# Kernel optimization log

Hardware: AMD Instinct MI355X
Metric: run time of the kernel (lower is better)

The kernel has to match this reference:

```python
import jax, jax.numpy as jnp
import numpy as np

KS = 2       # kernel_size (pad (0,1,0,1)+unfold only tiles to HxW for k=2)
L = 2        # num_attn_blocks
NH = 4       # n_heads
C = 128      # latent_dim
DH = C // NH
SCALE = 1.0 / float(np.sqrt(DH))


def _ln(x, eps=1e-6):
    m = jnp.mean(x, axis=-1, keepdims=True)
    v = jnp.var(x, axis=-1, keepdims=True)
    return (x - m) * jax.lax.rsqrt(v + eps)


def setup_inputs() -> dict:
    key = jax.random.key(0)
    ks = jax.random.split(key, 24)
    B, Hd, Wd, upf = 2, 64, 96, 2
    d = {
        'feat_map': jax.random.normal(ks[0], (B, C, Hd, Wd), jnp.float32),
        'feat_map_up': jax.random.normal(ks[1], (B, C, Hd * upf, Wd * upf), jnp.float32),
    }
    shapes = {'ctx_ln_b': (L, C), 'q_w': (L, C, C), 'q_b': (L, C), 'k_w': (L, C, C), 'k_b': (L, C),
              'v_w': (L, C, C), 'v_b': (L, C), 'o_w': (L, C, C), 'o_b': (L, C),
              'fc1_w': (L, C, 4 * C), 'fc1_b': (L, 4 * C), 'fc2_w': (L, 4 * C, C), 'fc2_b': (L, C),
              'out1_w': (3 * C, 3 * C), 'out1_b': (3 * C,), 'out2_w': (3 * C, 1), 'out2_b': (1,)}
    for i, (n, shp) in enumerate(shapes.items()):
        d[n] = jax.random.normal(ks[2 + i], shp, jnp.float32) * 0.02
    d['ctx_ln_g'] = jnp.ones((L, C), jnp.float32)
    d['upsample_factor'] = 2
    return d


def _forward(feat_map, feat_map_up, ctx_ln_g, ctx_ln_b, q_w, q_b, k_w, k_b, v_w, v_b,
             o_w, o_b, fc1_w, fc1_b, fc2_w, fc2_b, out1_w, out1_b, out2_w, out2_b, upf):
    B, _, Hd, Wd = feat_map.shape
    Hu, Wu = Hd * upf, Wd * upf
    N, K2 = B * Hu * Wu, KS * KS
    rh = jnp.minimum((jnp.arange(Hu) // upf)[:, None] + jnp.arange(KS)[None, :], Hd - 1)  # (Hu,KS)
    rw = jnp.minimum((jnp.arange(Wu) // upf)[:, None] + jnp.arange(KS)[None, :], Wd - 1)  # (Wu,KS)
    ctx = feat_map[:, :, rh][:, :, :, :, rw]                      # (B,C,Hu,KS,Wu,KS)
    ctx = jnp.transpose(ctx, (0, 2, 4, 3, 5, 1)).reshape(N, K2, C)  # (N,K2,C)
    # ALiBi bias: -L1(|up pixel coord - upf*down window coord|), separable in y/x
    dy = -jnp.abs(jnp.arange(Hu)[:, None] - rh * upf).astype(jnp.float32)  # (Hu,KS)
    dx = -jnp.abs(jnp.arange(Wu)[:, None] - rw * upf).astype(jnp.float32)  # (Wu,KS)
    cd = (dy[:, None, :, None] + dx[None, :, None, :]).reshape(Hu * Wu, K2)
    cd = jnp.tile(cd, (B, 1))                                     # (N,K2)
    x24 = 24.0 ** (1.0 / NH)
    slopes = 1.0 / x24 ** (jnp.arange(NH, dtype=jnp.float32) + 1.0)
    bias = slopes[None, :, None, None] * cd[:, None, None, :]     # (N,NH,1,K2)

    x = jnp.transpose(feat_map_up, (0, 2, 3, 1)).reshape(N, 1, C)
    for l in range(L):
        xn = _ln(x)
        cn = _ln(ctx, eps=1e-5) * ctx_ln_g[l] + ctx_ln_b[l]
        q = (xn @ q_w[l] + q_b[l]).reshape(N, 1, NH, DH).transpose(0, 2, 1, 3)
        k = (cn @ k_w[l] + k_b[l]).reshape(N, K2, NH, DH).transpose(0, 2, 1, 3)
        v = (cn @ v_w[l] + v_b[l]).reshape(N, K2, NH, DH).transpose(0, 2, 1, 3)
        sim = jnp.einsum('nhqd,nhkd->nhqk', q, k) * SCALE + bias
        attn = jax.nn.softmax(sim, axis=-1)
        o = jnp.einsum('nhqk,nhkd->nhqd', attn, v).transpose(0, 2, 1, 3).reshape(N, 1, C)
        x = x + o @ o_w[l] + o_b[l]
        h = _ln(x)
        x = x + jax.nn.gelu(h @ fc1_w[l] + fc1_b[l], approximate=True) @ fc2_w[l] + fc2_b[l]

    xf = _ln(x)      # (N,1,C)
    cf = _ln(ctx)    # (N,K2,C)
    fin = jnp.concatenate([jnp.broadcast_to(xf, (N, K2, C)), cf, xf - cf], axis=-1)  # (N,K2,3C)
    h1 = jax.nn.gelu(fin @ out1_w + out1_b, approximate=False)
    out = (h1 @ out2_w + out2_b).reshape(B, Hu, Wu, K2).transpose(0, 3, 1, 2)  # (B,K2,Hu,Wu)
    return jax.nn.softmax(out, axis=1)


def reference(feat_map, feat_map_up, ctx_ln_b, q_w, q_b, k_w, k_b, v_w, v_b, o_w, o_b,
              fc1_w, fc1_b, fc2_w, fc2_b, out1_w, out1_b, out2_w, out2_b, ctx_ln_g,
              upsample_factor):
    return _forward(feat_map, feat_map_up, ctx_ln_g, ctx_ln_b, q_w, q_b, k_w, k_b,
                    v_w, v_b, o_w, o_b, fc1_w, fc1_b, fc2_w, fc2_b,
                    out1_w, out1_b, out2_w, out2_b, upsample_factor)
```

## Files before the change

### kernel.cpp

```cpp
#include <hip/hip_runtime.h>
#include <math.h>

#define C_   128
#define HU_  128
#define WU_  192
#define HD_  64
#define WD_  96
#define HWD_ (HD_ * WD_)

typedef unsigned short u16;
typedef __attribute__((ext_vector_type(8))) short s8v;
typedef __attribute__((ext_vector_type(4))) float f4v;

#define OFF_Q   0
#define OFF_K   32768
#define OFF_V   65536
#define OFF_O   98304
#define OFF_F1  131072
#define OFF_F2  262144
#define OFF_XC  393216
#define OFF_CC  442368
#define OFF_NRM 491520
#define OFF_VB  2064384

#define SLOT 2176

__device__ __forceinline__ u16 f2bf(float f) {
    unsigned u = __float_as_uint(f);
    unsigned r = (u + 0x7FFFu + ((u >> 16) & 1u)) >> 16;
    return (u16)r;
}
__device__ __forceinline__ float bfu(u16 h) { return __uint_as_float(((unsigned)h) << 16); }

__device__ __forceinline__ float gelu_tanh(float x) {
    float u = 1.5957691216057308f * (x + 0.044715f * x * x * x);
    float e = __expf(u);
    float th = 1.0f - 2.0f / (1.0f + e);
    return 0.5f * x * (1.0f + th);
}
__device__ __forceinline__ float fast_erf(float x) {
    float z = fabsf(x);
    float t = 1.0f / (1.0f + 0.3275911f * z);
    float p = t * (0.254829592f + t * (-0.284496736f + t * (1.421413741f +
              t * (-1.453152027f + t * 1.061405429f))));
    float r = 1.0f - p * __expf(-z * z);
    return copysignf(r, x);
}
__device__ __forceinline__ float gelu_erf(float x) {
    return 0.5f * x * (1.0f + fast_erf(x * 0.7071067811865476f));
}

__device__ __forceinline__ void glds1(const u16* src, u16* dst, int lane) {
    __builtin_amdgcn_global_load_lds(
        (const __attribute__((address_space(1))) void*)(src + (size_t)lane * 8),
        (__attribute__((address_space(3))) void*)dst, 16, 0, 0);
}
#define WAITVM8() asm volatile("s_waitcnt vmcnt(8)" ::: "memory")
#define WAITVM6() asm volatile("s_waitcnt vmcnt(6)" ::: "memory")
#define WAITVM0() asm volatile("s_waitcnt vmcnt(0)" ::: "memory")

__global__ __launch_bounds__(256) void swz_all(
    const float* __restrict__ q_w, const float* __restrict__ k_w,
    const float* __restrict__ v_w, const float* __restrict__ o_w,
    const float* __restrict__ f1w, const float* __restrict__ f2w,
    const float* __restrict__ o1w,
    const float* __restrict__ ctx_g, const float* __restrict__ ctx_b,
    const float* __restrict__ vb_in, u16* __restrict__ ws)
{
    int tid = blockIdx.x * 256 + threadIdx.x;
    int f = tid >> 6, lane = tid & 63;
    if (f >= 964) return;
    if (f >= 960) {
        int lf = f - 960;
        int ly = lf >> 1, col = (lf & 1) * 64 + lane;
        float s = vb_in[ly * 128 + col];
        const float* bp = ctx_b + ly * 128;
        const float* wp = v_w + (size_t)ly * 128 * 128 + col;
        for (int c = 0; c < 128; ++c) s += bp[c] * wp[(size_t)c * 128];
        ((float*)(ws + OFF_VB))[ly * 128 + col] = s;
        return;
    }
    int rq = 8 * (lane >> 4), cq = lane & 15;
    const float* src; const float* src2 = nullptr; float sgn = 1.f;
    int NT, N, dstoff, lf;
    bool scale_g = false;
    if (f < 64)       { src = q_w;  NT = 8;  N = 128; dstoff = OFF_Q;  lf = f; }
    else if (f < 128) { src = k_w;  NT = 8;  N = 128; dstoff = OFF_K;  lf = f - 64;  scale_g = true; }
    else if (f < 192) { src = v_w;  NT = 8;  N = 128; dstoff = OFF_V;  lf = f - 128; scale_g = true; }
    else if (f < 256) { src = o_w;  NT = 8;  N = 128; dstoff = OFF_O;  lf = f - 192; }
    else if (f < 512) { src = f1w;  NT = 32; N = 512; dstoff = OFF_F1; lf = f - 256; }
    else if (f < 768) { src = f2w;  NT = 8;  N = 128; dstoff = OFF_F2; lf = f - 512; }
    else if (f < 864) { src = o1w;             src2 = o1w + 256 * 384; sgn =  1.f;
                        NT = 24; N = 384; dstoff = OFF_XC; lf = f - 768; }
    else              { src = o1w + 128 * 384; src2 = o1w + 256 * 384; sgn = -1.f;
                        NT = 24; N = 384; dstoff = OFF_CC; lf = f - 864; }
    int kt = lf / NT, nt = lf - kt * NT;
    int row0 = kt * 32 + rq, col = nt * 16 + cq;
    s8v o;
#pragma unroll
    for (int j = 0; j < 8; ++j) {
        float v = src[(size_t)(row0 + j) * N + col];
        if (src2) v += sgn * src2[(size_t)(row0 + j) * N + col];
        if (scale_g) v *= ctx_g[row0 + j];
        o[j] = (short)f2bf(v);
    }
    *(s8v*)(ws + dstoff + (size_t)lf * 512 + (size_t)lane * 8) = o;
}

__global__ __launch_bounds__(256) void norm_kernel(const float* __restrict__ fm,
                                                   u16* __restrict__ dst) {
    int row = blockIdx.x;
    int b = row >> 6, y = row & 63;
    __shared__ float tile[128 * 97];
    __shared__ float smean[96], srst[96];
    for (int idx = threadIdx.x; idx < 128 * 96; idx += 256) {
        int c = idx / 96, w = idx - c * 96;
        tile[c * 97 + w] = fm[(((size_t)b * 128 + c) * 64 + y) * 96 + w];
    }
    __syncthreads();
    if (threadIdx.x < 96) {
        int w = threadIdx.x;
        float s = 0.f, ss = 0.f;
        for (int c = 0; c < 128; ++c) { float v = tile[c * 97 + w]; s += v; ss += v * v; }
        float mn = s * (1.f / 128.f);
        smean[w] = mn;
        srst[w]  = rsqrtf(ss * (1.f / 128.f) - mn * mn + 1e-5f);
    }
    __syncthreads();
    for (int idx = threadIdx.x; idx < 96 * 16; idx += 256) {
        int w = idx >> 4, cg = idx & 15;
        float mn = smean[w], iv = srst[w];
        s8v o;
#pragma unroll
        for (int j = 0; j < 8; ++j)
            o[j] = (short)f2bf((tile[(8 * cg + j) * 97 + w] - mn) * iv);
        *(s8v*)(dst + ((size_t)row * 96 + w) * 128 + 8 * cg) = o;
    }
}

__global__ __launch_bounds__(64, 2) void fused_kernel(
    const u16*  __restrict__ nrmb, const float* __restrict__ fmu,
    const u16*  __restrict__ wsb,
    const float* __restrict__ qb, const float* __restrict__ ob,
    const float* __restrict__ f1b, const float* __restrict__ f2b,
    const float* __restrict__ o1b, const float* __restrict__ o2w,
    const float* __restrict__ o2b,
    float* __restrict__ out)
{
    const int lane = threadIdx.x;
    const int cidx = lane & 15, quad = lane >> 4;
    const int n0 = blockIdx.x * 16;
    const int b  = n0 / (HU_ * WU_);
    const int rem = n0 - b * (HU_ * WU_);
    const int hu  = rem / WU_;
    const int wu0 = rem - hu * WU_;

    __shared__ __align__(16) u16 wlds[2][4096];
    __shared__ u16 arena[2 * SLOT];
    __shared__ float s_at[272];
    float* s_rs = s_at;

    const float* vbp = (const float*)(wsb + OFF_VB);

    float xacc[8][4];
#pragma unroll
    for (int nt = 0; nt < 8; ++nt) {
        int ch = 16 * nt + cidx;
        float4 v = *(const float4*)(fmu + ((size_t)(b * C_ + ch) * HU_ + hu) * WU_ + wu0 + 4 * quad);
        xacc[nt][0] = v.x; xacc[nt][1] = v.y; xacc[nt][2] = v.z; xacc[nt][3] = v.w;
    }

    const float slopes[4] = {0.451801007f, 0.204124145f, 0.092223264f, 0.041666668f};
    const int ry0 = min(hu >> 1, HD_ - 1);
    const int ry1 = min((hu >> 1) + 1, HD_ - 1);
    const float dyv0 = -(float)abs(hu - 2 * ry0);
    const float dyv1 = -(float)abs(hu - 2 * ry1);

    const int k2l = cidx & 3;
    const int ryl = (k2l >> 1) ? ry1 : ry0;
    int cbase[4];
#pragma unroll
    for (int mt = 0; mt < 4; ++mt) {
        int p = 4 * mt + (cidx >> 2);
        int rxv = min(((wu0 + p) >> 1) + (k2l & 1), WD_ - 1);
        cbase[mt] = ((b * HD_ + ryl) * WD_ + rxv) * 128;
    }

#pragma unroll 1
    for (int ly = 0; ly < 2; ++ly) {
        const u16* Wq = wsb + OFF_Q  + ly * 16384;
        const u16* Wk = wsb + OFF_K  + ly * 16384;
        const u16* Wv = wsb + OFF_V  + ly * 16384;
        const u16* Wo = wsb + OFF_O  + ly * 16384;
        const u16* W1 = wsb + OFF_F1 + ly * 65536;
        const u16* W2 = wsb + OFF_F2 + ly * 65536;

        s8v fr[4][2];

#pragma unroll
        for (int jj = 0; jj < 8; ++jj) glds1(Wq + (size_t)jj * 512, &wlds[0][jj * 512], lane);
#pragma unroll
        for (int jj = 0; jj < 8; ++jj) glds1(Wq + (size_t)(8 + jj) * 512, &wlds[1][jj * 512], lane);

        {
            float mo[4], io[4];
#pragma unroll
            for (int r = 0; r < 4; ++r) {
                float s = 0.f, ss = 0.f;
#pragma unroll
                for (int nt = 0; nt < 8; ++nt) { float v = xacc[nt][r]; s += v; ss += v * v; }
#pragma unroll
                for (int m = 1; m <= 8; m <<= 1) { s += __shfl_xor(s, m, 64); ss += __shfl_xor(ss, m, 64); }
                float mn = s * (1.f / 128.f);
                mo[r] = mn; io[r] = rsqrtf(ss * (1.f / 128.f) - mn * mn + 1e-6f);
            }
#pragma unroll
            for (int nt = 0; nt < 8; ++nt)
#pragma unroll
                for (int r = 0; r < 4; ++r)
                    arena[(4 * quad + r) * 136 + 16 * nt + cidx] =
                        f2bf((xacc[nt][r] - mo[r]) * io[r]);
        }
        __syncthreads();
        s8v a_xn[4];
#pragma unroll
        for (int kt = 0; kt < 4; ++kt)
            a_xn[kt] = *(const s8v*)(arena + cidx * 136 + kt * 32 + 8 * quad);

        {
            f4v qa[8];
#pragma unroll
            for (int nt = 0; nt < 8; ++nt) {
                float bvv = qb[ly * C_ + 16 * nt + cidx];
                f4v t = {bvv, bvv, bvv, bvv}; qa[nt] = t;
            }
#pragma unroll
            for (int g = 0; g < 4; ++g) {
                if (g < 3) { WAITVM8(); } else { WAITVM0(); }
#pragma unroll
                for (int nt = 0; nt < 8; ++nt) {
                    s8v w = *(const s8v*)&wlds[g & 1][nt * 512 + lane * 8];
                    qa[nt] = __builtin_amdgcn_mfma_f32_16x16x32_bf16(a_xn[g], w, qa[nt], 0, 0, 0);
                }
                if (g < 2) {
#pragma unroll
                    for (int jj = 0; jj < 8; ++jj)
                        glds1(Wq + (size_t)((g + 2) * 8 + jj) * 512, &wlds[g & 1][jj * 512], lane);
                }
            }
#pragma unroll
            for (int kt = 0; kt < 4; ++kt)
#pragma unroll
                for (int i = 0; i < 2; ++i)
                    fr[kt][i] = *(const s8v*)(nrmb + cbase[i] + kt * 32 + 8 * quad);
#pragma unroll
            for (int jj = 0; jj < 8; ++jj)
                glds1(Wk + (size_t)(((jj & 3) * 8) + (jj >> 2)) * 512, &wlds[0][jj * 512], lane);
#pragma unroll
            for (int jj = 0; jj < 8; ++jj) {
                const int j = 8 + jj;
                glds1(Wk + (size_t)(((j & 3) * 8) + (j >> 2)) * 512, &wlds[1][jj * 512], lane);
            }
#pragma unroll
            for (int nt = 0; nt < 8; ++nt)
#pragma unroll
                for (int r = 0; r < 4; ++r)
                    arena[(4 * quad + r) * 136 + 16 * nt + cidx] = f2bf(qa[nt][r]);
        }
        __syncthreads();

#pragma unroll
        for (int g = 0; g < 8; ++g) {
            if (g < 7) { WAITVM8(); } else { WAITVM0(); }
            if (g == 4) {
#pragma unroll
                for (int kt = 0; kt < 4; ++kt)
#pragma unroll
                    for (int i = 0; i < 2; ++i)
                        fr[kt][i] = *(const s8v*)(nrmb + cbase[2 + i] + kt * 32 + 8 * quad);
            }
            const int mh = g >> 2, h = g & 3;
            float part[2][4];
#pragma unroll
            for (int i = 0; i < 2; ++i)
#pragma unroll
                for (int r = 0; r < 4; ++r) part[i][r] = 0.f;
#pragma unroll
            for (int ntp = 0; ntp < 2; ++ntp) {
                const int nt = 2 * h + ntp;
                f4v ka[2];
#pragma unroll
                for (int i = 0; i < 2; ++i) { f4v t = {0.f, 0.f, 0.f, 0.f}; ka[i] = t; }
#pragma unroll
                for (int kt = 0; kt < 4; ++kt) {
                    s8v w = *(const s8v*)&wlds[g & 1][(ntp * 4 + kt) * 512 + lane * 8];
                    ka[0] = __builtin_amdgcn_mfma_f32_16x16x32_bf16(fr[kt][0], w, ka[0], 0, 0, 0);
                    ka[1] = __builtin_amdgcn_mfma_f32_16x16x32_bf16(fr[kt][1], w, ka[1], 0, 0, 0);
                }
#pragma unroll
                for (int i = 0; i < 2; ++i) {
                    float qv = bfu(arena[(4 * (2 * mh + i) + quad) * 136 + 16 * nt + cidx]);
#pragma unroll
                    for (int r = 0; r < 4; ++r) part[i][r] = fmaf(qv, ka[i][r], part[i][r]);
                }
            }
#pragma unroll
            for (int i = 0; i < 2; ++i)
#pragma unroll
                for (int r = 0; r < 4; ++r) {
#pragma unroll
                    for (int m = 1; m <= 8; m <<= 1) part[i][r] += __shfl_xor(part[i][r], m, 64);
                }
            if (cidx == 0) {
#pragma unroll
                for (int i = 0; i < 2; ++i) {
                    float4 t = {part[i][0], part[i][1], part[i][2], part[i][3]};
                    *(float4*)&s_at[(4 * (2 * mh + i) + quad) * 16 + 4 * h] = t;
                }
            }
            if (g < 6) {
                const int gn = g + 2;
#pragma unroll
                for (int jj = 0; jj < 8; ++jj) {
                    const int j = 8 * (gn & 3) + jj;
                    glds1(Wk + (size_t)(((j & 3) * 8) + (j >> 2)) * 512, &wlds[g & 1][jj * 512], lane);
                }
            }
        }
#pragma unroll
        for (int kt = 0; kt < 4; ++kt)
#pragma unroll
            for (int i = 0; i < 2; ++i)
                fr[kt][i] = *(const s8v*)(nrmb + cbase[i] + kt * 32 + 8 * quad);
#pragma unroll
        for (int jj = 0; jj < 8; ++jj)
            glds1(Wv + (size_t)(((jj & 3) * 8) + (jj >> 2)) * 512, &wlds[0][jj * 512], lane);
#pragma unroll
        for (int jj = 0; jj < 8; ++jj)
            glds1(Wv + (size_t)(((jj & 3) * 8) + 2 + (jj >> 2)) * 512, &wlds[1][jj * 512], lane);
        __syncthreads();

        {
            int p = lane >> 2, h = lane & 3;
            float4 sc = *(float4*)&s_at[p * 16 + 4 * h];
            int pw = wu0 + p;
            float sim[4] = {sc.x, sc.y, sc.z, sc.w};
#pragma unroll
            for (int r = 0; r < 4; ++r) {
                int rxv = min((pw >> 1) + (r & 1), WD_ - 1);
                float cd = ((r >> 1) ? dyv1 : dyv0) - (float)abs(pw - 2 * rxv);
                sim[r] = sim[r] * 0.17677669529663687f + slopes[h] * cd;
            }
            float mx = fmaxf(fmaxf(sim[0], sim[1]), fmaxf(sim[2], sim[3]));
            float e0 = __expf(sim[0] - mx), e1 = __expf(sim[1] - mx);
            float e2 = __expf(sim[2] - mx), e3 = __expf(sim[3] - mx);
            float si = 1.f / (e0 + e1 + e2 + e3);
            float4 at = {e0 * si, e1 * si, e2 * si, e3 * si};
            *(float4*)&s_at[p * 16 + 4 * h] = at;
        }
        __syncthreads();

#pragma unroll
        for (int g = 0; g < 8; ++g) {
            if (g < 7) { WAITVM8(); } else { WAITVM0(); }
            if (g == 4) {
#pragma unroll
                for (int kt = 0; kt < 4; ++kt)
#pragma unroll
                    for (int i = 0; i < 2; ++i)
                        fr[kt][i] = *(const s8v*)(nrmb + cbase[2 + i] + kt * 32 + 8 * quad);
            }
            const int mh = g >> 2, gp = g & 3;
#pragma unroll
            for (int ntp = 0; ntp < 2; ++ntp) {
                const int nt = 2 * gp + ntp;
                float vbb = vbp[ly * C_ + 16 * nt + cidx];
                f4v va[2];
#pragma unroll
                for (int i = 0; i < 2; ++i) { f4v t = {vbb, vbb, vbb, vbb}; va[i] = t; }
#pragma unroll
                for (int kt = 0; kt < 4; ++kt) {
                    s8v w = *(const s8v*)&wlds[g & 1][(ntp * 4 + kt) * 512 + lane * 8];
                    va[0] = __builtin_amdgcn_mfma_f32_16x16x32_bf16(fr[kt][0], w, va[0], 0, 0, 0);
                    va[1] = __builtin_amdgcn_mfma_f32_16x16x32_bf16(fr[kt][1], w, va[1], 0, 0, 0);
                }
                const int h = nt >> 1;
#pragma unroll
                for (int i = 0; i < 2; ++i) {
                    const int mt = 2 * mh + i;
                    float4 at = *(float4*)&s_at[(4 * mt + quad) * 16 + 4 * h];
                    float ov = at.x * va[i][0] + at.y * va[i][1] + at.z * va[i][2] + at.w * va[i][3];
                    arena[(4 * mt + quad) * 136 + 16 * nt + cidx] = f2bf(ov);
                }
            }
            if (g < 6) {
                const int gq = (g + 2) & 3;
#pragma unroll
                for (int jj = 0; jj < 8; ++jj)
                    glds1(Wv + (size_t)(((jj & 3) * 8) + 2 * gq + (jj >> 2)) * 512, &wlds[g & 1][jj * 512], lane);
            }
        }
#pragma unroll
        for (int jj = 0; jj < 8; ++jj) glds1(Wo + (size_t)jj * 512, &wlds[0][jj * 512], lane);
#pragma unroll
        for (int jj = 0; jj < 8; ++jj) glds1(Wo + (size_t)(8 + jj) * 512, &wlds[1][jj * 512], lane);
        __syncthreads();

        {
            s8v a_o[4];
#pragma unroll
            for (int kt = 0; kt < 4; ++kt)
                a_o[kt] = *(const s8v*)(arena + cidx * 136 + kt * 32 + 8 * quad);
            f4v oa[8];
#pragma unroll
            for (int nt = 0; nt < 8; ++nt) {
                float bvv = ob[ly * C_ + 16 * nt + cidx];
                f4v t = {bvv, bvv, bvv, bvv}; oa[nt] = t;
            }
#pragma unroll
            for (int g = 0; g < 4; ++g) {
                if (g < 3) { WAITVM8(); } else { WAITVM0(); }
#pragma unroll
                for (int nt = 0; nt < 8; ++nt) {
                    s8v w = *(const s8v*)&wlds[g & 1][nt * 512 + lane * 8];
                    oa[nt] = __builtin_amdgcn_mfma_f32_16x16x32_bf16(a_o[g], w, oa[nt], 0, 0, 0);
                }
                if (g < 2) {
#pragma unroll
                    for (int jj = 0; jj < 8; ++jj)
                        glds1(Wo + (size_t)((g + 2) * 8 + jj) * 512, &wlds[g & 1][jj * 512], lane);
                }
            }
#pragma unroll
            for (int jj = 0; jj < 8; ++jj) glds1(W1 + (size_t)jj * 512, &wlds[0][jj * 512], lane);
#pragma unroll
            for (int jj = 0; jj < 8; ++jj) glds1(W1 + (size_t)(32 + jj) * 512, &wlds[1][jj * 512], lane);
#pragma unroll
            for (int nt = 0; nt < 8; ++nt)
#pragma unroll
                for (int r = 0; r < 4; ++r) xacc[nt][r] += oa[nt][r];
        }
        __syncthreads();

        {
            float mo[4], io[4];
#pragma unroll
            for (int r = 0; r < 4; ++r) {
                float s = 0.f, ss = 0.f;
#pragma unroll
                for (int nt = 0; nt < 8; ++nt) { float v = xacc[nt][r]; s += v; ss += v * v; }
#pragma unroll
                for (int m = 1; m <= 8; m <<= 1) { s += __shfl_xor(s, m, 64); ss += __shfl_xor(ss, m, 64); }
                float mn = s * (1.f / 128.f);
                mo[r] = mn; io[r] = rsqrtf(ss * (1.f / 128.f) - mn * mn + 1e-6f);
            }
#pragma unroll
            for (int nt = 0; nt < 8; ++nt)
#pragma unroll
                for (int r = 0; r < 4; ++r)
                    arena[(4 * quad + r) * 136 + 16 * nt + cidx] =
                        f2bf((xacc[nt][r] - mo[r]) * io[r]);
        }
        __syncthreads();
        s8v a_hn[4];
#pragma unroll
        for (int kt = 0; kt < 4; ++kt)
            a_hn[kt] = *(const s8v*)(arena + cidx * 136 + kt * 32 + 8 * quad);

        {
            f4v ga[8];
#pragma unroll
            for (int nt = 0; nt < 8; ++nt) {
                float bvv = f2b[ly * C_ + 16 * nt + cidx];
                f4v t = {bvv, bvv, bvv, bvv}; ga[nt] = t;
            }
#pragma unroll 1
            for (int c = 0; c < 4; ++c) {
                f4v fa[8];
#pragma unroll
                for (int nt = 0; nt < 8; ++nt) {
                    float bvv = f1b[ly * 512 + 128 * c + 16 * nt + cidx];
                    f4v t = {bvv, bvv, bvv, bvv}; fa[nt] = t;
                }
#pragma unroll
                for (int g = 0; g < 4; ++g) {
                    if (g < 3) { WAITVM8(); } else { WAITVM0(); }
#pragma unroll
                    for (int nt = 0; nt < 8; ++nt) {
                        s8v w = *(const s8v*)&wlds[g & 1][nt * 512 + lane * 8];
                        fa[nt] = __builtin_amdgcn_mfma_f32_16x16x32_bf16(a_hn[g], w, fa[nt], 0, 0, 0);
                    }
                    if (g < 2) {
#pragma unroll
                        for (int jj = 0; jj < 8; ++jj)
                            glds1(W1 + (size_t)((g + 2) * 32 + 8 * c + jj) * 512, &wlds[g & 1][jj * 512], lane);
                    }
                }
#pragma unroll
                for (int jj = 0; jj < 8; ++jj)
                    glds1(W2 + (size_t)(32 * c + jj) * 512, &wlds[0][jj * 512], lane);
#pragma unroll
                for (int jj = 0; jj < 8; ++jj)
                    glds1(W2 + (size_t)(32 * c + 8 + jj) * 512, &wlds[1][jj * 512], lane);
#pragma unroll
                for (int nt = 0; nt < 8; ++nt)
#pragma unroll
                    for (int r = 0; r < 4; ++r)
                        arena[SLOT + (4 * quad + r) * 136 + 16 * nt + cidx] =
                            f2bf(gelu_tanh(fa[nt][r]));
                __syncthreads();
#pragma unroll
                for (int g = 0; g < 4; ++g) {
                    if (g < 3) { WAITVM8(); } else { WAITVM0(); }
                    s8v a = *(const s8v*)(arena + SLOT + cidx * 136 + g * 32 + 8 * quad);
#pragma unroll
                    for (int nt = 0; nt < 8; ++nt) {
                        s8v w = *(const s8v*)&wlds[g & 1][nt * 512 + lane * 8];
                        ga[nt] = __builtin_amdgcn_mfma_f32_16x16x32_bf16(a, w, ga[nt], 0, 0, 0);
                    }
                    if (g < 2) {
#pragma unroll
                        for (int jj = 0; jj < 8; ++jj)
                            glds1(W2 + (size_t)(32 * c + (g + 2) * 8 + jj) * 512, &wlds[g & 1][jj * 512], lane);
                    }
                }
                if (c < 3) {
#pragma unroll
                    for (int jj = 0; jj < 8; ++jj)
                        glds1(W1 + (size_t)(8 * (c + 1) + jj) * 512, &wlds[0][jj * 512], lane);
#pragma unroll
                    for (int jj = 0; jj < 8; ++jj)
                        glds1(W1 + (size_t)(32 + 8 * (c + 1) + jj) * 512, &wlds[1][jj * 512], lane);
                }
                __syncthreads();
            }
#pragma unroll
            for (int nt = 0; nt < 8; ++nt)
#pragma unroll
                for (int r = 0; r < 4; ++r) xacc[nt][r] += ga[nt][r];
        }
    }

    const u16* Wxc = wsb + OFF_XC;
    const u16* Wcc = wsb + OFF_CC;
#pragma unroll
    for (int jj = 0; jj < 6; ++jj)
        glds1(Wxc + (size_t)((jj / 3) * 24 + (jj % 3)) * 512, &wlds[0][jj * 512], lane);
#pragma unroll
    for (int jj = 0; jj < 6; ++jj)
        glds1(Wxc + (size_t)((2 + jj / 3) * 24 + (jj % 3)) * 512, &wlds[1][jj * 512], lane);
    {
        float mo[4], io[4];
#pragma unroll
        for (int r = 0; r < 4; ++r) {
            float s = 0.f, ss = 0.f;
#pragma unroll
            for (int nt = 0; nt < 8; ++nt) { float v = xacc[nt][r]; s += v; ss += v * v; }
#pragma unroll
            for (int m = 1; m <= 8; m <<= 1) { s += __shfl_xor(s, m, 64); ss += __shfl_xor(ss, m, 64); }
            float mn = s * (1.f / 128.f);
            mo[r] = mn; io[r] = rsqrtf(ss * (1.f / 128.f) - mn * mn + 1e-6f);
        }
#pragma unroll
        for (int nt = 0; nt < 8; ++nt)
#pragma unroll
            for (int r = 0; r < 4; ++r)
                arena[(4 * quad + r) * 136 + 16 * nt + cidx] =
                    f2bf((xacc[nt][r] - mo[r]) * io[r]);
    }
    __syncthreads();
    s8v a_xf[4];
#pragma unroll
    for (int kt = 0; kt < 4; ++kt)
        a_xf[kt] = *(const s8v*)(arena + cidx * 136 + kt * 32 + 8 * quad);

    float part[4][4];
#pragma unroll
    for (int mt = 0; mt < 4; ++mt)
#pragma unroll
        for (int r = 0; r < 4; ++r) part[mt][r] = 0.f;

#pragma unroll 1
    for (int it = 0; it < 8; ++it) {
        const int nbase = 6 * (it >> 1) + 3 * (it & 1);
        {
            f4v hx[3];
#pragma unroll
            for (int ntl = 0; ntl < 3; ++ntl) {
                float hb = o1b[16 * (nbase + ntl) + cidx];
                f4v t = {hb, hb, hb, hb}; hx[ntl] = t;
            }
            WAITVM6();
#pragma unroll
            for (int kt = 0; kt < 2; ++kt)
#pragma unroll
                for (int ntl = 0; ntl < 3; ++ntl) {
                    s8v w = *(const s8v*)&wlds[0][(kt * 3 + ntl) * 512 + lane * 8];
                    hx[ntl] = __builtin_amdgcn_mfma_f32_16x16x32_bf16(a_xf[kt], w, hx[ntl], 0, 0, 0);
                }
            WAITVM0();
#pragma unroll
            for (int kt = 2; kt < 4; ++kt)
#pragma unroll
                for (int ntl = 0; ntl < 3; ++ntl) {
                    s8v w = *(const s8v*)&wlds[1][((kt - 2) * 3 + ntl) * 512 + lane * 8];
                    hx[ntl] = __builtin_amdgcn_mfma_f32_16x16x32_bf16(a_xf[kt], w, hx[ntl], 0, 0, 0);
                }
            if (it < 7) {
                const int nb2 = 6 * ((it + 1) >> 1) + 3 * ((it + 1) & 1);
#pragma unroll
                for (int jj = 0; jj < 6; ++jj)
                    glds1(Wxc + (size_t)((jj / 3) * 24 + nb2 + (jj % 3)) * 512, &wlds[0][jj * 512], lane);
#pragma unroll
                for (int jj = 0; jj < 6; ++jj)
                    glds1(Wxc + (size_t)((2 + jj / 3) * 24 + nb2 + (jj % 3)) * 512, &wlds[1][jj * 512], lane);
            }
#pragma unroll
            for (int ntl = 0; ntl < 3; ++ntl)
#pragma unroll
                for (int r = 0; r < 4; ++r)
                    arena[SLOT + (4 * quad + r) * 56 + 16 * ntl + cidx] = f2bf(hx[ntl][r]);
        }
        __syncthreads();

        f4v hc[3][4];
#pragma unroll
        for (int ntl = 0; ntl < 3; ++ntl)
#pragma unroll
            for (int mt = 0; mt < 4; ++mt) { f4v t = {0.f, 0.f, 0.f, 0.f}; hc[ntl][mt] = t; }
#pragma unroll 1
        for (int kt = 0; kt < 4; ++kt) {
            s8v frh[4];
#pragma unroll
            for (int mt = 0; mt < 4; ++mt)
                frh[mt] = *(const s8v*)(nrmb + cbase[mt] + kt * 32 + 8 * quad);
#pragma unroll
            for (int ntl = 0; ntl < 3; ++ntl) {
                s8v w = *(const s8v*)(Wcc + ((size_t)((kt * 24 + nbase + ntl) * 64 + lane)) * 8);
#pragma unroll
                for (int mt = 0; mt < 4; ++mt)
                    hc[ntl][mt] = __builtin_amdgcn_mfma_f32_16x16x32_bf16(frh[mt], w, hc[ntl][mt], 0, 0, 0);
            }
        }

#pragma unroll
        for (int ntl = 0; ntl < 3; ++ntl) {
            float w2v = o2w[16 * (nbase + ntl) + cidx];
#pragma unroll
            for (int mt = 0; mt < 4; ++mt)
#pragma unroll
                for (int r = 0; r < 4; ++r) {
                    float h1 = hc[ntl][mt][r] +
                               bfu(arena[SLOT + (4 * mt + quad) * 56 + 16 * ntl + cidx]);
                    part[mt][r] = fmaf(gelu_erf(h1), w2v, part[mt][r]);
                }
        }
        __syncthreads();
    }

#pragma unroll
    for (int mt = 0; mt < 4; ++mt)
#pragma unroll
        for (int r = 0; r < 4; ++r) {
#pragma unroll
            for (int m = 1; m <= 8; m <<= 1) part[mt][r] += __shfl_xor(part[mt][r], m, 64);
            part[mt][r] += o2b[0];
        }
    if (cidx == 0) {
#pragma unroll
        for (int mt = 0; mt < 4; ++mt) {
            float4 t = {part[mt][0], part[mt][1], part[mt][2], part[mt][3]};
            *(float4*)&s_rs[(4 * mt + quad) * 4] = t;
        }
    }
    __syncthreads();

    if (lane < 16) {
        int p = lane;
        float4 vv = *(float4*)&s_rs[4 * p];
        float mx = fmaxf(fmaxf(vv.x, vv.y), fmaxf(vv.z, vv.w));
        float e0 = __expf(vv.x - mx), e1 = __expf(vv.y - mx);
        float e2 = __expf(vv.z - mx), e3 = __expf(vv.w - mx);
        float si = 1.f / (e0 + e1 + e2 + e3);
        size_t base = ((size_t)(b * 4) * HU_ + hu) * WU_ + wu0 + p;
        out[base]                          = e0 * si;
        out[base + (size_t)HU_ * WU_]      = e1 * si;
        out[base + (size_t)2 * HU_ * WU_]  = e2 * si;
        out[base + (size_t)3 * HU_ * WU_]  = e3 * si;
    }
}

extern "C" void kernel_launch(void* const* d_in, const int* in_sizes, int n_in,
                              void* d_out, int out_size, void* d_ws, size_t ws_size,
                              hipStream_t stream) {
    const float* feat_map    = (const float*)d_in[0];
    const float* feat_map_up = (const float*)d_in[1];
    const float* ctx_ln_b    = (const float*)d_in[2];
    const float* q_w  = (const float*)d_in[3];
    const float* q_b  = (const float*)d_in[4];
    const float* k_w  = (const float*)d_in[5];
    const float* v_w  = (const float*)d_in[7];
    const float* v_b  = (const float*)d_in[8];
    const float* o_w  = (const float*)d_in[9];
    const float* o_b  = (const float*)d_in[10];
    const float* fc1_w = (const float*)d_in[11];
    const float* fc1_b = (const float*)d_in[12];
    const float* fc2_w = (const float*)d_in[13];
    const float* fc2_b = (const float*)d_in[14];
    const float* out1_w = (const float*)d_in[15];
    const float* out1_b = (const float*)d_in[16];
    const float* out2_w = (const float*)d_in[17];
    const float* out2_b = (const float*)d_in[18];
    const float* ctx_ln_g = (const float*)d_in[19];
    float* out = (float*)d_out;
    u16* ws = (u16*)d_ws;

    swz_all<<<242, 256, 0, stream>>>(q_w, k_w, v_w, o_w, fc1_w, fc2_w, out1_w,
                                     ctx_ln_g, ctx_ln_b, v_b, ws);
    norm_kernel<<<128, 256, 0, stream>>>(feat_map, ws + OFF_NRM);

    fused_kernel<<<3072, 64, 0, stream>>>(
        ws + OFF_NRM, feat_map_up, ws,
        q_b, o_b, fc1_b, fc2_b,
        out1_b, out2_w, out2_b, out);
}
```

Measured before the change: 414.4 us.

## Share staged weight tiles across two waves per block with split cooperative loads

The fused kernel now runs two wavefronts per block, each handling its own 16 pixels. The wavefronts share the double-buffered weight tiles in LDS, and each wave issues half of the global-to-LDS weight loads. Per-wave scratch arenas stay private, so block-wide __syncthreads are replaced by lgkmcnt fences plus explicit s_barrier calls around the shared weight-buffer handoff. This halves per-pixel weight staging traffic and LDS footprint per pixel. The cost is inter-wave barrier coupling and fewer outstanding loads per wave.

```diff
diff --git a/kernel.cpp b/kernel.cpp
--- a/kernel.cpp
+++ b/kernel.cpp
@@ -55,9 +55,11 @@
         (const __attribute__((address_space(1))) void*)(src + (size_t)lane * 8),
         (__attribute__((address_space(3))) void*)dst, 16, 0, 0);
 }
-#define WAITVM8() asm volatile("s_waitcnt vmcnt(8)" ::: "memory")
-#define WAITVM6() asm volatile("s_waitcnt vmcnt(6)" ::: "memory")
-#define WAITVM0() asm volatile("s_waitcnt vmcnt(0)" ::: "memory")
+#define GW4() do { asm volatile("s_waitcnt vmcnt(4)" ::: "memory"); __builtin_amdgcn_s_barrier(); } while (0)
+#define GW3() do { asm volatile("s_waitcnt vmcnt(3)" ::: "memory"); __builtin_amdgcn_s_barrier(); } while (0)
+#define GW0() do { asm volatile("s_waitcnt vmcnt(0)" ::: "memory"); __builtin_amdgcn_s_barrier(); } while (0)
+#define BAR() __builtin_amdgcn_s_barrier()
+#define WFENCE() asm volatile("s_waitcnt lgkmcnt(0)" ::: "memory")
 
 __global__ __launch_bounds__(256) void swz_all(
     const float* __restrict__ q_w, const float* __restrict__ k_w,
@@ -138,7 +140,7 @@
     }
 }
 
-__global__ __launch_bounds__(64, 2) void fused_kernel(
+__global__ __launch_bounds__(128, 2) void fused_kernel(
     const u16*  __restrict__ nrmb, const float* __restrict__ fmu,
     const u16*  __restrict__ wsb,
     const float* __restrict__ qb, const float* __restrict__ ob,
@@ -147,18 +149,22 @@
     const float* __restrict__ o2b,
     float* __restrict__ out)
 {
-    const int lane = threadIdx.x;
+    const int tid  = threadIdx.x;
+    const int wid  = tid >> 6;
+    const int lane = tid & 63;
     const int cidx = lane & 15, quad = lane >> 4;
-    const int n0 = blockIdx.x * 16;
+    const int n0 = blockIdx.x * 32 + wid * 16;
     const int b  = n0 / (HU_ * WU_);
     const int rem = n0 - b * (HU_ * WU_);
     const int hu  = rem / WU_;
     const int wu0 = rem - hu * WU_;
 
     __shared__ __align__(16) u16 wlds[2][4096];
-    __shared__ u16 arena[2 * SLOT];
-    __shared__ float s_at[272];
-    float* s_rs = s_at;
+    __shared__ __align__(16) u16 arena2[2][2 * SLOT];
+    __shared__ float s_at2[2][272];
+    u16*   const arena = arena2[wid];
+    float* const s_at  = s_at2[wid];
+    float* const s_rs  = s_at;
 
     const float* vbp = (const float*)(wsb + OFF_VB);
 
@@ -198,9 +204,15 @@
         s8v fr[4][2];
 
 #pragma unroll
-        for (int jj = 0; jj < 8; ++jj) glds1(Wq + (size_t)jj * 512, &wlds[0][jj * 512], lane);
-#pragma unroll
-        for (int jj = 0; jj < 8; ++jj) glds1(Wq + (size_t)(8 + jj) * 512, &wlds[1][jj * 512], lane);
+        for (int jl = 0; jl < 4; ++jl) {
+            int j = 4 * wid + jl;
+            glds1(Wq + (size_t)j * 512, &wlds[0][j * 512], lane);
+        }
+#pragma unroll
+        for (int jl = 0; jl < 4; ++jl) {
+            int j = 4 * wid + jl;
+            glds1(Wq + (size_t)(8 + j) * 512, &wlds[1][j * 512], lane);
+        }
 
         {
             float mo[4], io[4];
@@ -221,7 +233,7 @@
                     arena[(4 * quad + r) * 136 + 16 * nt + cidx] =
                         f2bf((xacc[nt][r] - mo[r]) * io[r]);
         }
-        __syncthreads();
+        WFENCE();
         s8v a_xn[4];
 #pragma unroll
         for (int kt = 0; kt < 4; ++kt)
@@ -236,16 +248,19 @@
             }
 #pragma unroll
             for (int g = 0; g < 4; ++g) {
-                if (g < 3) { WAITVM8(); } else { WAITVM0(); }
+                if (g < 3) { GW4(); } else { GW0(); }
 #pragma unroll
                 for (int nt = 0; nt < 8; ++nt) {
                     s8v w = *(const s8v*)&wlds[g & 1][nt * 512 + lane * 8];
                     qa[nt] = __builtin_amdgcn_mfma_f32_16x16x32_bf16(a_xn[g], w, qa[nt], 0, 0, 0);
                 }
+                BAR();
                 if (g < 2) {
 #pragma unroll
-                    for (int jj = 0; jj < 8; ++jj)
-                        glds1(Wq + (size_t)((g + 2) * 8 + jj) * 512, &wlds[g & 1][jj * 512], lane);
+                    for (int jl = 0; jl < 4; ++jl) {
+                        int j = 4 * wid + jl;
+                        glds1(Wq + (size_t)((g + 2) * 8 + j) * 512, &wlds[g & 1][j * 512], lane);
+                    }
                 }
             }
 #pragma unroll
@@ -254,12 +269,15 @@
                 for (int i = 0; i < 2; ++i)
                     fr[kt][i] = *(const s8v*)(nrmb + cbase[i] + kt * 32 + 8 * quad);
 #pragma unroll
-            for (int jj = 0; jj < 8; ++jj)
-                glds1(Wk + (size_t)(((jj & 3) * 8) + (jj >> 2)) * 512, &wlds[0][jj * 512], lane);
-#pragma unroll
-            for (int jj = 0; jj < 8; ++jj) {
-                const int j = 8 + jj;
-                glds1(Wk + (size_t)(((j & 3) * 8) + (j >> 2)) * 512, &wlds[1][jj * 512], lane);
+            for (int jl = 0; jl < 4; ++jl) {
+                int j = 4 * wid + jl;
+                glds1(Wk + (size_t)(((j & 3) * 8) + (j >> 2)) * 512, &wlds[0][j * 512], lane);
+            }
+#pragma unroll
+            for (int jl = 0; jl < 4; ++jl) {
+                int j = 4 * wid + jl;
+                int jc = 8 + j;
+                glds1(Wk + (size_t)(((jc & 3) * 8) + (jc >> 2)) * 512, &wlds[1][j * 512], lane);
             }
 #pragma unroll
             for (int nt = 0; nt < 8; ++nt)
@@ -267,11 +285,11 @@
                 for (int r = 0; r < 4; ++r)
                     arena[(4 * quad + r) * 136 + 16 * nt + cidx] = f2bf(qa[nt][r]);
         }
-        __syncthreads();
+        WFENCE();
 
 #pragma unroll
         for (int g = 0; g < 8; ++g) {
-            if (g < 7) { WAITVM8(); } else { WAITVM0(); }
+            if (g < 7) { GW4(); } else { GW0(); }
             if (g == 4) {
 #pragma unroll
                 for (int kt = 0; kt < 4; ++kt)
@@ -318,12 +336,14 @@
                     *(float4*)&s_at[(4 * (2 * mh + i) + quad) * 16 + 4 * h] = t;
                 }
             }
+            BAR();
             if (g < 6) {
                 const int gn = g + 2;
 #pragma unroll
-                for (int jj = 0; jj < 8; ++jj) {
-                    const int j = 8 * (gn & 3) + jj;
-                    glds1(Wk + (size_t)(((j & 3) * 8) + (j >> 2)) * 512, &wlds[g & 1][jj * 512], lane);
+                for (int jl = 0; jl < 4; ++jl) {
+                    int j = 4 * wid + jl;
+                    int jc = 8 * (gn & 3) + j;
+                    glds1(Wk + (size_t)(((jc & 3) * 8) + (jc >> 2)) * 512, &wlds[g & 1][j * 512], lane);
                 }
             }
         }
@@ -333,12 +353,16 @@
             for (int i = 0; i < 2; ++i)
                 fr[kt][i] = *(const s8v*)(nrmb + cbase[i] + kt * 32 + 8 * quad);
 #pragma unroll
-        for (int jj = 0; jj < 8; ++jj)
-            glds1(Wv + (size_t)(((jj & 3) * 8) + (jj >> 2)) * 512, &wlds[0][jj * 512], lane);
-#pragma unroll
-        for (int jj = 0; jj < 8; ++jj)
-            glds1(Wv + (size_t)(((jj & 3) * 8) + 2 + (jj >> 2)) * 512, &wlds[1][jj * 512], lane);
-        __syncthreads();
+        for (int jl = 0; jl < 4; ++jl) {
+            int j = 4 * wid + jl;
+            glds1(Wv + (size_t)(((j & 3) * 8) + (j >> 2)) * 512, &wlds[0][j * 512], lane);
+        }
+#pragma unroll
+        for (int jl = 0; jl < 4; ++jl) {
+            int j = 4 * wid + jl;
+            glds1(Wv + (size_t)(((j & 3) * 8) + 2 + (j >> 2)) * 512, &wlds[1][j * 512], lane);
+        }
+        WFENCE();
 
         {
             int p = lane >> 2, h = lane & 3;
@@ -358,11 +382,11 @@
             float4 at = {e0 * si, e1 * si, e2 * si, e3 * si};
             *(float4*)&s_at[p * 16 + 4 * h] = at;
         }
-        __syncthreads();
+        WFENCE();
 
 #pragma unroll
         for (int g = 0; g < 8; ++g) {
-            if (g < 7) { WAITVM8(); } else { WAITVM0(); }
+            if (g < 7) { GW4(); } else { GW0(); }
             if (g == 4) {
 #pragma unroll
                 for (int kt = 0; kt < 4; ++kt)
@@ -393,18 +417,27 @@
                     arena[(4 * mt + quad) * 136 + 16 * nt + cidx] = f2bf(ov);
                 }
             }
+            BAR();
             if (g < 6) {
                 const int gq = (g + 2) & 3;
 #pragma unroll
-                for (int jj = 0; jj < 8; ++jj)
-                    glds1(Wv + (size_t)(((jj & 3) * 8) + 2 * gq + (jj >> 2)) * 512, &wlds[g & 1][jj * 512], lane);
-            }
-        }
-#pragma unroll
-        for (int jj = 0; jj < 8; ++jj) glds1(Wo + (size_t)jj * 512, &wlds[0][jj * 512], lane);
-#pragma unroll
-        for (int jj = 0; jj < 8; ++jj) glds1(Wo + (size_t)(8 + jj) * 512, &wlds[1][jj * 512], lane);
-        __syncthreads();
+                for (int jl = 0; jl < 4; ++jl) {
+                    int j = 4 * wid + jl;
+                    glds1(Wv + (size_t)(((j & 3) * 8) + 2 * gq + (j >> 2)) * 512, &wlds[g & 1][j * 512], lane);
+                }
+            }
+        }
+#pragma unroll
+        for (int jl = 0; jl < 4; ++jl) {
+            int j = 4 * wid + jl;
+            glds1(Wo + (size_t)j * 512, &wlds[0][j * 512], lane);
+        }
+#pragma unroll
+        for (int jl = 0; jl < 4; ++jl) {
+            int j = 4 * wid + jl;
+            glds1(Wo + (size_t)(8 + j) * 512, &wlds[1][j * 512], lane);
+        }
+        WFENCE();
 
         {
             s8v a_o[4];
@@ -419,28 +452,36 @@
             }
 #pragma unroll
             for (int g = 0; g < 4; ++g) {
-                if (g < 3) { WAITVM8(); } else { WAITVM0(); }
+                if (g < 3) { GW4(); } else { GW0(); }
 #pragma unroll
                 for (int nt = 0; nt < 8; ++nt) {
                     s8v w = *(const s8v*)&wlds[g & 1][nt * 512 + lane * 8];
                     oa[nt] = __builtin_amdgcn_mfma_f32_16x16x32_bf16(a_o[g], w, oa[nt], 0, 0, 0);
                 }
+                BAR();
                 if (g < 2) {
 #pragma unroll
-                    for (int jj = 0; jj < 8; ++jj)
-                        glds1(Wo + (size_t)((g + 2) * 8 + jj) * 512, &wlds[g & 1][jj * 512], lane);
-                }
-            }
-#pragma unroll
-            for (int jj = 0; jj < 8; ++jj) glds1(W1 + (size_t)jj * 512, &wlds[0][jj * 512], lane);
-#pragma unroll
-            for (int jj = 0; jj < 8; ++jj) glds1(W1 + (size_t)(32 + jj) * 512, &wlds[1][jj * 512], lane);
+                    for (int jl = 0; jl < 4; ++jl) {
+                        int j = 4 * wid + jl;
+                        glds1(Wo + (size_t)((g + 2) * 8 + j) * 512, &wlds[g & 1][j * 512], lane);
+                    }
+                }
+            }
+#pragma unroll
+            for (int jl = 0; jl < 4; ++jl) {
+                int j = 4 * wid + jl;
+                glds1(W1 + (size_t)j * 512, &wlds[0][j * 512], lane);
+            }
+#pragma unroll
+            for (int jl = 0; jl < 4; ++jl) {
+                int j = 4 * wid + jl;
+                glds1(W1 + (size_t)(32 + j) * 512, &wlds[1][j * 512], lane);
+            }
 #pragma unroll
             for (int nt = 0; nt < 8; ++nt)
 #pragma unroll
                 for (int r = 0; r < 4; ++r) xacc[nt][r] += oa[nt][r];
         }
-        __syncthreads();
 
         {
             float mo[4], io[4];
@@ -461,7 +502,7 @@
                     arena[(4 * quad + r) * 136 + 16 * nt + cidx] =
                         f2bf((xacc[nt][r] - mo[r]) * io[r]);
         }
-        __syncthreads();
+        WFENCE();
         s8v a_hn[4];
 #pragma unroll
         for (int kt = 0; kt < 4; ++kt)
@@ -484,55 +525,68 @@
                 }
 #pragma unroll
                 for (int g = 0; g < 4; ++g) {
-                    if (g < 3) { WAITVM8(); } else { WAITVM0(); }
+                    if (g < 3) { GW4(); } else { GW0(); }
 #pragma unroll
                     for (int nt = 0; nt < 8; ++nt) {
                         s8v w = *(const s8v*)&wlds[g & 1][nt * 512 + lane * 8];
                         fa[nt] = __builtin_amdgcn_mfma_f32_16x16x32_bf16(a_hn[g], w, fa[nt], 0, 0, 0);
                     }
+                    BAR();
                     if (g < 2) {
 #pragma unroll
-                        for (int jj = 0; jj < 8; ++jj)
-                            glds1(W1 + (size_t)((g + 2) * 32 + 8 * c + jj) * 512, &wlds[g & 1][jj * 512], lane);
+                        for (int jl = 0; jl < 4; ++jl) {
+                            int j = 4 * wid + jl;
+                            glds1(W1 + (size_t)((g + 2) * 32 + 8 * c + j) * 512, &wlds[g & 1][j * 512], lane);
+                        }
                     }
                 }
 #pragma unroll
-                for (int jj = 0; jj < 8; ++jj)
-                    glds1(W2 + (size_t)(32 * c + jj) * 512, &wlds[0][jj * 512], lane);
-#pragma unroll
-                for (int jj = 0; jj < 8; ++jj)
-                    glds1(W2 + (size_t)(32 * c + 8 + jj) * 512, &wlds[1][jj * 512], lane);
+                for (int jl = 0; jl < 4; ++jl) {
+                    int j = 4 * wid + jl;
+                    glds1(W2 + (size_t)(32 * c + j) * 512, &wlds[0][j * 512], lane);
+                }
+#pragma unroll
+                for (int jl = 0; jl < 4; ++jl) {
+                    int j = 4 * wid + jl;
+                    glds1(W2 + (size_t)(32 * c + 8 + j) * 512, &wlds[1][j * 512], lane);
+                }
 #pragma unroll
                 for (int nt = 0; nt < 8; ++nt)
 #pragma unroll
                     for (int r = 0; r < 4; ++r)
                         arena[SLOT + (4 * quad + r) * 136 + 16 * nt + cidx] =
                             f2bf(gelu_tanh(fa[nt][r]));
-                __syncthreads();
+                WFENCE();
 #pragma unroll
                 for (int g = 0; g < 4; ++g) {
-                    if (g < 3) { WAITVM8(); } else { WAITVM0(); }
+                    if (g < 3) { GW4(); } else { GW0(); }
                     s8v a = *(const s8v*)(arena + SLOT + cidx * 136 + g * 32 + 8 * quad);
 #pragma unroll
                     for (int nt = 0; nt < 8; ++nt) {
                         s8v w = *(const s8v*)&wlds[g & 1][nt * 512 + lane * 8];
                         ga[nt] = __builtin_amdgcn_mfma_f32_16x16x32_bf16(a, w, ga[nt], 0, 0, 0);
                     }
+                    BAR();
                     if (g < 2) {
 #pragma unroll
-                        for (int jj = 0; jj < 8; ++jj)
-                            glds1(W2 + (size_t)(32 * c + (g + 2) * 8 + jj) * 512, &wlds[g & 1][jj * 512], lane);
+                        for (int jl = 0; jl < 4; ++jl) {
+                            int j = 4 * wid + jl;
+                            glds1(W2 + (size_t)(32 * c + (g + 2) * 8 + j) * 512, &wlds[g & 1][j * 512], lane);
+                        }
                     }
                 }
                 if (c < 3) {
 #pragma unroll
-                    for (int jj = 0; jj < 8; ++jj)
-                        glds1(W1 + (size_t)(8 * (c + 1) + jj) * 512, &wlds[0][jj * 512], lane);
-#pragma unroll
-                    for (int jj = 0; jj < 8; ++jj)
-                        glds1(W1 + (size_t)(32 + 8 * (c + 1) + jj) * 512, &wlds[1][jj * 512], lane);
-                }
-                __syncthreads();
+                    for (int jl = 0; jl < 4; ++jl) {
+                        int j = 4 * wid + jl;
+                        glds1(W1 + (size_t)(8 * (c + 1) + j) * 512, &wlds[0][j * 512], lane);
+                    }
+#pragma unroll
+                    for (int jl = 0; jl < 4; ++jl) {
+                        int j = 4 * wid + jl;
+                        glds1(W1 + (size_t)(32 + 8 * (c + 1) + j) * 512, &wlds[1][j * 512], lane);
+                    }
+                }
             }
 #pragma unroll
             for (int nt = 0; nt < 8; ++nt)
@@ -544,11 +598,15 @@
     const u16* Wxc = wsb + OFF_XC;
     const u16* Wcc = wsb + OFF_CC;
 #pragma unroll
-    for (int jj = 0; jj < 6; ++jj)
-        glds1(Wxc + (size_t)((jj / 3) * 24 + (jj % 3)) * 512, &wlds[0][jj * 512], lane);
-#pragma unroll
-    for (int jj = 0; jj < 6; ++jj)
-        glds1(Wxc + (size_t)((2 + jj / 3) * 24 + (jj % 3)) * 512, &wlds[1][jj * 512], lane);
+    for (int jl = 0; jl < 3; ++jl) {
+        int j = 3 * wid + jl;
+        glds1(Wxc + (size_t)((j / 3) * 24 + (j % 3)) * 512, &wlds[0][j * 512], lane);
+    }
+#pragma unroll
+    for (int jl = 0; jl < 3; ++jl) {
+        int j = 3 * wid + jl;
+        glds1(Wxc + (size_t)((2 + j / 3) * 24 + (j % 3)) * 512, &wlds[1][j * 512], lane);
+    }
     {
         float mo[4], io[4];
 #pragma unroll
@@ -568,7 +626,7 @@
                 arena[(4 * quad + r) * 136 + 16 * nt + cidx] =
                     f2bf((xacc[nt][r] - mo[r]) * io[r]);
     }
-    __syncthreads();
+    WFENCE();
     s8v a_xf[4];
 #pragma unroll
     for (int kt = 0; kt < 4; ++kt)
@@ -590,7 +648,7 @@
                 float hb = o1b[16 * (nbase + ntl) + cidx];
                 f4v t = {hb, hb, hb, hb}; hx[ntl] = t;
             }
-            WAITVM6();
+            GW3();
 #pragma unroll
             for (int kt = 0; kt < 2; ++kt)
 #pragma unroll
@@ -598,7 +656,7 @@
                     s8v w = *(const s8v*)&wlds[0][(kt * 3 + ntl) * 512 + lane * 8];
                     hx[ntl] = __builtin_amdgcn_mfma_f32_16x16x32_bf16(a_xf[kt], w, hx[ntl], 0, 0, 0);
                 }
-            WAITVM0();
+            GW0();
 #pragma unroll
             for (int kt = 2; kt < 4; ++kt)
 #pragma unroll
@@ -606,14 +664,19 @@
                     s8v w = *(const s8v*)&wlds[1][((kt - 2) * 3 + ntl) * 512 + lane * 8];
                     hx[ntl] = __builtin_amdgcn_mfma_f32_16x16x32_bf16(a_xf[kt], w, hx[ntl], 0, 0, 0);
                 }
+            BAR();
             if (it < 7) {
                 const int nb2 = 6 * ((it + 1) >> 1) + 3 * ((it + 1) & 1);
 #pragma unroll
-                for (int jj = 0; jj < 6; ++jj)
-                    glds1(Wxc + (size_t)((jj / 3) * 24 + nb2 + (jj % 3)) * 512, &wlds[0][jj * 512], lane);
-#pragma unroll
-                for (int jj = 0; jj < 6; ++jj)
-                    glds1(Wxc + (size_t)((2 + jj / 3) * 24 + nb2 + (jj % 3)) * 512, &wlds[1][jj * 512], lane);
+                for (int jl = 0; jl < 3; ++jl) {
+                    int j = 3 * wid + jl;
+                    glds1(Wxc + (size_t)((j / 3) * 24 + nb2 + (j % 3)) * 512, &wlds[0][j * 512], lane);
+                }
+#pragma unroll
+                for (int jl = 0; jl < 3; ++jl) {
+                    int j = 3 * wid + jl;
+                    glds1(Wxc + (size_t)((2 + j / 3) * 24 + nb2 + (j % 3)) * 512, &wlds[1][j * 512], lane);
+                }
             }
 #pragma unroll
             for (int ntl = 0; ntl < 3; ++ntl)
@@ -621,7 +684,7 @@
                 for (int r = 0; r < 4; ++r)
                     arena[SLOT + (4 * quad + r) * 56 + 16 * ntl + cidx] = f2bf(hx[ntl][r]);
         }
-        __syncthreads();
+        WFENCE();
 
         f4v hc[3][4];
 #pragma unroll
@@ -655,7 +718,7 @@
                     part[mt][r] = fmaf(gelu_erf(h1), w2v, part[mt][r]);
                 }
         }
-        __syncthreads();
+        WFENCE();
     }
 
 #pragma unroll
@@ -673,7 +736,7 @@
             *(float4*)&s_rs[(4 * mt + quad) * 4] = t;
         }
     }
-    __syncthreads();
+    WFENCE();
 
     if (lane < 16) {
         int p = lane;
@@ -719,7 +782,7 @@
                                      ctx_ln_g, ctx_ln_b, v_b, ws);
     norm_kernel<<<128, 256, 0, stream>>>(feat_map, ws + OFF_NRM);
 
-    fused_kernel<<<3072, 64, 0, stream>>>(
+    fused_kernel<<<1536, 128, 0, stream>>>(
         ws + OFF_NRM, feat_map_up, ws,
         q_b, o_b, fc1_b, fc2_b,
         out1_b, out2_w, out2_b, out);
```

Measured after the change: 412.6 us. Within noise of the previous version (-0.4%).
